# Kernel tuning notes

Hardware: AMD Instinct MI355X
Metric: run time of the kernel (lower is better)

## Reference

```python
import jax, jax.numpy as jnp
import numpy as np

N = 50000      # n_nodes
E = 800000     # n_edges (nnz)
F = 256        # n_features
H = 256        # architecture (GCN hidden)
K = 16         # n_clusters
CLUSTER_REG = 1.0
CON_REG = 1.0


def setup_inputs() -> dict:
    key = jax.random.key(0)
    ks = jax.random.split(key, 12)
    inp = {
        "edge_src": jax.random.randint(ks[0], (E,), 0, N, dtype=jnp.int32),
        "edge_dst": jax.random.randint(ks[1], (E,), 0, N, dtype=jnp.int32),
        "edge_w_norm": jax.random.uniform(ks[2], (E,), dtype=jnp.float32),
        "features": jax.random.normal(ks[3], (N, F), dtype=jnp.float32),
        "aug_features": jax.random.normal(ks[4], (N, F), dtype=jnp.float32),
        # GCN encoder params (Linear no-bias + additive bias per DGI-style GCN)
        "W1": jax.random.normal(ks[5], (F, H), dtype=jnp.float32) / np.sqrt(F),
        "b1": jnp.zeros((H,), dtype=jnp.float32),
        # student GCN params
        "Ws": jax.random.normal(ks[6], (H, K), dtype=jnp.float32) / np.sqrt(H),
        "bs": jnp.zeros((K,), dtype=jnp.float32),
        # teacher GCN params (EMA copy; fixed here)
        "Wt": jax.random.normal(ks[7], (H, K), dtype=jnp.float32) / np.sqrt(H),
        "bt": jnp.zeros((K,), dtype=jnp.float32),
        "n_nodes": N,
    }
    return inp


def _spmm(w, src, dst, X, n):
    # (sparse A) @ X with A given as COO (src=row, dst=col, w=value)
    return jax.ops.segment_sum(w[:, None] * X[dst], src, num_segments=n)


def _gcn(X, W, b, w, src, dst, n):
    # act(spmm(A_norm, X @ W) + b) with act = selu
    return jax.nn.selu(_spmm(w, src, dst, X @ W, n) + b)


def _normalize(x):
    # F.normalize(x, dim=-1, p=2)
    nrm = jnp.sqrt(jnp.sum(x * x, axis=-1, keepdims=True))
    return x / jnp.maximum(nrm, 1e-12)


def reference(edge_src, edge_dst, edge_w_norm, features, aug_features,
              W1, b1, Ws, bs, Wt, bt, n_nodes):
    n = features.shape[0]
    n_edges = edge_src.shape[0]

    # encoder + student assignments
    gcn_out = _gcn(features, W1, b1, edge_w_norm, edge_src, edge_dst, n)
    logits = _spmm(edge_w_norm, edge_src, edge_dst, gcn_out @ Ws, n) + bs
    assignments = jax.nn.softmax(jax.nn.selu(logits), axis=1)  # [N, K]

    # degrees = torch.sparse.sum(graph, dim=0) (binary adjacency values)
    ones_e = jnp.ones((n_edges,), dtype=features.dtype)
    degrees = jax.ops.segment_sum(ones_e, edge_dst, num_segments=n)[:, None]  # [N,1]

    # graph_pooled = (A @ S).T @ S  (A values are all 1)
    AS = jax.ops.segment_sum(assignments[edge_dst], edge_src, num_segments=n)
    graph_pooled = AS.T @ assignments  # [K, K]

    normalizer_left = assignments.T @ degrees          # [K, 1]
    normalizer = (normalizer_left @ normalizer_left.T) / 2.0 / n_edges
    spectral_loss = -jnp.trace(graph_pooled - normalizer) / 2.0 / n_edges

    cluster_sizes = jnp.sum(assignments, axis=0)
    cluster_loss = (jnp.linalg.norm(cluster_sizes) / n_nodes * np.sqrt(float(K)) - 1.0)
    cluster_loss = cluster_loss * CLUSTER_REG

    # teacher branch (no grad)
    g2 = _gcn(aug_features, W1, b1, edge_w_norm, edge_src, edge_dst, n)
    t_logits = _spmm(edge_w_norm, edge_src, edge_dst, g2 @ Wt, n) + bt
    assignments_hat = jax.lax.stop_gradient(
        jax.nn.softmax(jax.nn.selu(t_logits), axis=-1))

    con = jnp.mean(2.0 - 2.0 * jnp.sum(_normalize(assignments_hat) * _normalize(assignments), axis=-1))

    loss = spectral_loss + cluster_loss + CON_REG * con
    return loss
```

## Files before the change

kernel.cpp:

```cpp
#include <hip/hip_runtime.h>
#include <math.h>

constexpr int Fdim = 256;
constexpr int Hdim = 256;
constexpr int Kc   = 16;

constexpr int RSTRIDE = 32;
constexpr int NRED    = 34;
constexpr int BCAP    = 5120;

typedef __attribute__((ext_vector_type(8))) short s8v;
typedef __attribute__((ext_vector_type(4))) float f4v;

__device__ __forceinline__ float selu1(float x){
    const float scale = 1.0507009873554805f;
    const float alpha = 1.6732632423543772f;
    return scale * (x > 0.f ? x : alpha * expm1f(x));
}

__device__ __forceinline__ ushort f2bf(float x){
    union { float f; unsigned u; } c; c.f = x;
    unsigned r = c.u + 0x7fffu + ((c.u >> 16) & 1u);
    return (ushort)(r >> 16);
}

__device__ __forceinline__ float bflo(unsigned v){
    union { unsigned u; float f; } c; c.u = v << 16; return c.f;
}
__device__ __forceinline__ float bfhi(unsigned v){
    union { unsigned u; float f; } c; c.u = v & 0xffff0000u; return c.f;
}

__device__ __forceinline__ unsigned char f2fp8(float x){
    int v = __builtin_amdgcn_cvt_pk_fp8_f32(x, x, 0, false);
    return (unsigned char)(v & 0xff);
}

__global__ __launch_bounds__(256) void prep_kernel(
        const float* __restrict__ W1, ushort* __restrict__ WT,
        const float* __restrict__ Ws, const float* __restrict__ Wt,
        ushort* __restrict__ WsT, ushort* __restrict__ WtT){
    __shared__ float tbuf[16][17];
    int b = blockIdx.x;
    int t = threadIdx.x;
    if (b < 256){
        int bx = b & 15, by = b >> 4;
        int tx = t & 15, ty = t >> 4;
        int k  = by * 16 + ty;
        int nn = bx * 16 + tx;
        tbuf[ty][tx] = W1[k * 256 + nn];
        __syncthreads();
        int n2 = bx * 16 + ty;
        int k2 = by * 16 + tx;
        WT[n2 * 256 + k2] = f2bf(tbuf[tx][ty]);
    } else {
        int h = t;
        #pragma unroll
        for (int c = 0; c < 16; ++c){
            WsT[c * 256 + h] = f2bf(Ws[h * 16 + c]);
            WtT[c * 256 + h] = f2bf(Wt[h * 16 + c]);
        }
    }
}

__global__ __launch_bounds__(256, 2) void mega_kernel(
        const int* __restrict__ esrc, const int* __restrict__ edst,
        const float* __restrict__ ew, int* __restrict__ bcnt,
        int* __restrict__ bsrc, uint2* __restrict__ bdw, int E, int nbuck,
        const float* __restrict__ A0, const float* __restrict__ A1,
        const ushort* __restrict__ Bt, unsigned char* __restrict__ C8,
        int M, int nrt){
    __shared__ char smem[32768];
    int tid = threadIdx.x;

    if (blockIdx.x < 256){
        int* hist = (int*)smem;
        int* base = hist + 256;
        int* cur  = base + 256;
        int chunk = (E + 255) / 256;
        int lo = blockIdx.x * chunk;
        int hi = min(lo + chunk, E);
        hist[tid] = 0;
        __syncthreads();
        for (int i = lo + tid; i < hi; i += 256)
            atomicAdd(&hist[esrc[i] >> 8], 1);
        __syncthreads();
        if (tid < nbuck && hist[tid] > 0)
            base[tid] = atomicAdd(&bcnt[tid * 32], hist[tid]);
        cur[tid] = 0;
        __syncthreads();
        for (int i = lo + tid; i < hi; i += 256){
            int s = esrc[i], d = edst[i];
            float wv = ew[i];
            int b = s >> 8;
            int p = base[b] + atomicAdd(&cur[b], 1);
            if (p < BCAP){
                bsrc[(size_t)b * BCAP + p] = s;
                bdw[(size_t)b * BCAP + p]  = make_uint2((unsigned)d, __float_as_uint(wv));
            }
        }
        return;
    }

    ushort* blds = (ushort*)smem;
    int gid = blockIdx.x - 256;
    int z   = gid / (2 * nrt);
    int rem = gid - z * (2 * nrt);
    int by  = rem >> 1;
    int bx  = rem & 1;
    int n0  = bx * 128;
    int bm  = by * 128;
    const float* A = z ? A1 : A0;
    int halfoff = z * 256;

    int w = tid >> 6, l = tid & 63;
    int lr = l & 15, lk = l >> 4;

    int r0 = bm + w * 32 + lr;
    int r1 = r0 + 16;
    int rc0 = min(r0, M - 1), rc1 = min(r1, M - 1);

    f4v acc[2][8];
    #pragma unroll
    for (int m = 0; m < 2; ++m)
        #pragma unroll
        for (int t = 0; t < 8; ++t)
            acc[m][t] = (f4v){0.f, 0.f, 0.f, 0.f};

    for (int kp = 0; kp < 2; ++kp){
        #pragma unroll
        for (int j = 0; j < 8; ++j){
            int c  = j * 256 + tid;
            int nl = c >> 4, kc = c & 15;
            uint4 v = *reinterpret_cast<const uint4*>(
                Bt + (((size_t)(n0 + nl)) << 8) + kp * 128 + (kc << 3));
            unsigned boff = (unsigned)(((nl << 8) + (kc << 4)) ^ ((nl & 7) << 4));
            *reinterpret_cast<uint4*>(reinterpret_cast<char*>(blds) + boff) = v;
        }

        const float* a0 = A + (size_t)rc0 * 256 + kp * 128 + lk * 8;
        const float* a1 = A + (size_t)rc1 * 256 + kp * 128 + lk * 8;
        s8v af0[4], af1[4];
        #pragma unroll
        for (int ks = 0; ks < 4; ++ks){
            float4 x0 = *reinterpret_cast<const float4*>(a0 + ks * 32);
            float4 x1 = *reinterpret_cast<const float4*>(a0 + ks * 32 + 4);
            af0[ks][0] = (short)f2bf(x0.x); af0[ks][1] = (short)f2bf(x0.y);
            af0[ks][2] = (short)f2bf(x0.z); af0[ks][3] = (short)f2bf(x0.w);
            af0[ks][4] = (short)f2bf(x1.x); af0[ks][5] = (short)f2bf(x1.y);
            af0[ks][6] = (short)f2bf(x1.z); af0[ks][7] = (short)f2bf(x1.w);
            float4 y0 = *reinterpret_cast<const float4*>(a1 + ks * 32);
            float4 y1 = *reinterpret_cast<const float4*>(a1 + ks * 32 + 4);
            af1[ks][0] = (short)f2bf(y0.x); af1[ks][1] = (short)f2bf(y0.y);
            af1[ks][2] = (short)f2bf(y0.z); af1[ks][3] = (short)f2bf(y0.w);
            af1[ks][4] = (short)f2bf(y1.x); af1[ks][5] = (short)f2bf(y1.y);
            af1[ks][6] = (short)f2bf(y1.z); af1[ks][7] = (short)f2bf(y1.w);
        }
        __syncthreads();

        #pragma unroll
        for (int ks = 0; ks < 4; ++ks){
            #pragma unroll
            for (int t = 0; t < 8; ++t){
                int nl = t * 16 + lr;
                unsigned boff = (unsigned)(((nl << 8) + ((ks * 4 + lk) << 4)) ^ ((nl & 7) << 4));
                s8v bf = *reinterpret_cast<const s8v*>(reinterpret_cast<const char*>(blds) + boff);
                acc[0][t] = __builtin_amdgcn_mfma_f32_16x16x32_bf16(af0[ks], bf, acc[0][t], 0, 0, 0);
                acc[1][t] = __builtin_amdgcn_mfma_f32_16x16x32_bf16(af1[ks], bf, acc[1][t], 0, 0, 0);
            }
        }
        if (kp == 0) __syncthreads();
    }

    #pragma unroll
    for (int m = 0; m < 2; ++m){
        #pragma unroll
        for (int t = 0; t < 8; ++t){
            int col = n0 + t * 16 + lr;
            #pragma unroll
            for (int j = 0; j < 4; ++j){
                int row = bm + w * 32 + m * 16 + lk * 4 + j;
                if (row < M) C8[(size_t)row * 512 + halfoff + col] = f2fp8(acc[m][t][j]);
            }
        }
    }
}

__global__ __launch_bounds__(256) void csr_build_kernel(
        const int* __restrict__ bcnt,
        const int* __restrict__ bsrc, const uint2* __restrict__ bdw,
        int* __restrict__ roff, uint2* __restrict__ csr, int n, int nbuck){
    __shared__ int sb[256];
    __shared__ int hist[256];
    __shared__ int loc[256];
    __shared__ int cur[256];
    int b = blockIdx.x, t = threadIdx.x;

    int vb = (t < nbuck) ? min(bcnt[t * 32], BCAP) : 0;
    sb[t] = vb;
    __syncthreads();
    for (int off = 1; off < 256; off <<= 1){
        int x = (t >= off) ? sb[t - off] : 0;
        __syncthreads();
        sb[t] += x;
        __syncthreads();
    }
    if (b == 0 && t == 0) roff[n] = sb[nbuck - 1];
    int cnt  = min(bcnt[b * 32], BCAP);
    int base = sb[b] - cnt;
    __syncthreads();

    hist[t] = 0;
    __syncthreads();
    for (int i = t; i < cnt; i += 256)
        atomicAdd(&hist[bsrc[(size_t)b * BCAP + i] & 255], 1);
    __syncthreads();
    int v = hist[t];
    loc[t] = v;
    __syncthreads();
    for (int off = 1; off < 256; off <<= 1){
        int x = (t >= off) ? loc[t - off] : 0;
        __syncthreads();
        loc[t] += x;
        __syncthreads();
    }
    int gi = b * 256 + t;
    if (gi < n) roff[gi] = base + loc[t] - v;
    cur[t] = 0;
    __syncthreads();
    for (int i = t; i < cnt; i += 256){
        int s   = bsrc[(size_t)b * BCAP + i];
        int idx = s & 255;
        int p = base + (loc[idx] - hist[idx]) + atomicAdd(&cur[idx], 1);
        csr[p] = bdw[(size_t)b * BCAP + i];
    }
}

__global__ __launch_bounds__(256) void spmm_h2_kernel(
        const unsigned char* __restrict__ XWp,
        const int* __restrict__ roff, const uint2* __restrict__ csr,
        const float* __restrict__ b1,
        ushort* __restrict__ Gs, ushort* __restrict__ Gt, int n){
    int wid = threadIdx.x >> 6, lane = threadIdx.x & 63;
    int r = blockIdx.x * 4 + wid;
    if (r >= n) return;
    int half = lane >> 5;
    int hl   = lane & 31;
    const unsigned char* base = XWp + lane * 8;
    int e0 = roff[r], e1 = roff[r + 1];
    float acc[8] = {};

    #define ACCUM8(V, W) do{                                                      \
        auto fa_ = __builtin_amdgcn_cvt_pk_f32_fp8((V).x, false);                 \
        acc[0] = fmaf((W), fa_[0], acc[0]); acc[1] = fmaf((W), fa_[1], acc[1]);   \
        auto fb_ = __builtin_amdgcn_cvt_pk_f32_fp8((V).x, true);                  \
        acc[2] = fmaf((W), fb_[0], acc[2]); acc[3] = fmaf((W), fb_[1], acc[3]);   \
        auto fc_ = __builtin_amdgcn_cvt_pk_f32_fp8((V).y, false);                 \
        acc[4] = fmaf((W), fc_[0], acc[4]); acc[5] = fmaf((W), fc_[1], acc[5]);   \
        auto fd_ = __builtin_amdgcn_cvt_pk_f32_fp8((V).y, true);                  \
        acc[6] = fmaf((W), fd_[0], acc[6]); acc[7] = fmaf((W), fd_[1], acc[7]);   \
    }while(0)

    int e = e0;
    for (; e + 7 < e1; e += 8){
        uint2 c0 = csr[e],     c1 = csr[e + 1];
        uint2 c2 = csr[e + 2], c3 = csr[e + 3];
        uint2 c4 = csr[e + 4], c5 = csr[e + 5];
        uint2 c6 = csr[e + 6], c7 = csr[e + 7];
        uint2 v0 = *reinterpret_cast<const uint2*>(base + ((size_t)c0.x << 9));
        uint2 v1 = *reinterpret_cast<const uint2*>(base + ((size_t)c1.x << 9));
        uint2 v2 = *reinterpret_cast<const uint2*>(base + ((size_t)c2.x << 9));
        uint2 v3 = *reinterpret_cast<const uint2*>(base + ((size_t)c3.x << 9));
        uint2 v4 = *reinterpret_cast<const uint2*>(base + ((size_t)c4.x << 9));
        uint2 v5 = *reinterpret_cast<const uint2*>(base + ((size_t)c5.x << 9));
        uint2 v6 = *reinterpret_cast<const uint2*>(base + ((size_t)c6.x << 9));
        uint2 v7 = *reinterpret_cast<const uint2*>(base + ((size_t)c7.x << 9));
        ACCUM8(v0, __uint_as_float(c0.y)); ACCUM8(v1, __uint_as_float(c1.y));
        ACCUM8(v2, __uint_as_float(c2.y)); ACCUM8(v3, __uint_as_float(c3.y));
        ACCUM8(v4, __uint_as_float(c4.y)); ACCUM8(v5, __uint_as_float(c5.y));
        ACCUM8(v6, __uint_as_float(c6.y)); ACCUM8(v7, __uint_as_float(c7.y));
    }
    for (; e + 3 < e1; e += 4){
        uint2 c0 = csr[e],     c1 = csr[e + 1];
        uint2 c2 = csr[e + 2], c3 = csr[e + 3];
        uint2 v0 = *reinterpret_cast<const uint2*>(base + ((size_t)c0.x << 9));
        uint2 v1 = *reinterpret_cast<const uint2*>(base + ((size_t)c1.x << 9));
        uint2 v2 = *reinterpret_cast<const uint2*>(base + ((size_t)c2.x << 9));
        uint2 v3 = *reinterpret_cast<const uint2*>(base + ((size_t)c3.x << 9));
        ACCUM8(v0, __uint_as_float(c0.y)); ACCUM8(v1, __uint_as_float(c1.y));
        ACCUM8(v2, __uint_as_float(c2.y)); ACCUM8(v3, __uint_as_float(c3.y));
    }
    for (; e < e1; ++e){
        uint2 c = csr[e];
        uint2 v = *reinterpret_cast<const uint2*>(base + ((size_t)c.x << 9));
        ACCUM8(v, __uint_as_float(c.y));
    }
    #undef ACCUM8

    const float* bp = b1 + hl * 8;
    float4 bb0 = *reinterpret_cast<const float4*>(bp);
    float4 bb1 = *reinterpret_cast<const float4*>(bp + 4);
    float bv[8] = {bb0.x, bb0.y, bb0.z, bb0.w, bb1.x, bb1.y, bb1.z, bb1.w};
    ushort o[8];
    #pragma unroll
    for (int q = 0; q < 8; ++q) o[q] = f2bf(selu1(acc[q] + bv[q]));
    uint4 ov = *reinterpret_cast<const uint4*>(o);
    ushort* gout = (half ? Gt : Gs) + (size_t)r * Hdim + hl * 8;
    *reinterpret_cast<uint4*>(gout) = ov;
}

__global__ __launch_bounds__(256) void gemm_k2_kernel(
        const ushort* __restrict__ Gs, const ushort* __restrict__ Gt,
        const ushort* __restrict__ WsT, const ushort* __restrict__ WtT,
        unsigned* __restrict__ GSp, int n){
    int wv = blockIdx.x * 4 + (threadIdx.x >> 6);
    int l  = threadIdx.x & 63;
    int lr = l & 15, lk = l >> 4;
    int nw = (n + 15) >> 4;
    if (wv >= nw) return;
    int r0 = wv * 16;

    s8v bs_[8], bt_[8];
    #pragma unroll
    for (int ks = 0; ks < 8; ++ks){
        bs_[ks] = *reinterpret_cast<const s8v*>(WsT + lr * 256 + ks * 32 + lk * 8);
        bt_[ks] = *reinterpret_cast<const s8v*>(WtT + lr * 256 + ks * 32 + lk * 8);
    }

    f4v accs = (f4v){0.f,0.f,0.f,0.f}, acct = (f4v){0.f,0.f,0.f,0.f};
    int row = min(r0 + lr, n - 1);
    const ushort* gsrow = Gs + (size_t)row * 256 + lk * 8;
    const ushort* gtrow = Gt + (size_t)row * 256 + lk * 8;
    #pragma unroll
    for (int ks = 0; ks < 8; ++ks){
        s8v a_s = *reinterpret_cast<const s8v*>(gsrow + ks * 32);
        s8v a_t = *reinterpret_cast<const s8v*>(gtrow + ks * 32);
        accs = __builtin_amdgcn_mfma_f32_16x16x32_bf16(a_s, bs_[ks], accs, 0, 0, 0);
        acct = __builtin_amdgcn_mfma_f32_16x16x32_bf16(a_t, bt_[ks], acct, 0, 0, 0);
    }
    #pragma unroll
    for (int j = 0; j < 4; ++j){
        int rr = r0 + lk * 4 + j;
        if (rr < n){
            unsigned pv = (unsigned)f2bf(accs[j]) | ((unsigned)f2bf(acct[j]) << 16);
            GSp[(size_t)rr * 16 + lr] = pv;
        }
    }
}

__global__ __launch_bounds__(256) void spmm_k2_kernel(
        const unsigned* __restrict__ GSp,
        const int* __restrict__ roff, const uint2* __restrict__ csr,
        const float* __restrict__ bsv, const float* __restrict__ btv,
        float* __restrict__ asg, float* __restrict__ red, int n){
    int tid  = threadIdx.x;
    int wid  = tid >> 6, lane = tid & 63;
    int slot = lane >> 4, j = lane & 15;
    float bs_ = bsv[j], bt_ = btv[j];
    float cs_l = 0.f, con_l = 0.f;

    int rstride = gridDim.x * 4;
    for (int r = blockIdx.x * 4 + wid; r < n; r += rstride){
        int e0 = roff[r], e1 = roff[r + 1];
        float as_ = 0.f, at_ = 0.f;
        for (int e = e0 + slot; e < e1; e += 4){
            uint2 c = csr[e];
            float w = __uint_as_float(c.y);
            unsigned v = GSp[(size_t)c.x * 16 + j];
            as_ = fmaf(w, bflo(v), as_);
            at_ = fmaf(w, bfhi(v), at_);
        }
        as_ += __shfl_xor(as_, 16); as_ += __shfl_xor(as_, 32);
        at_ += __shfl_xor(at_, 16); at_ += __shfl_xor(at_, 32);
        float xs = selu1(as_ + bs_);
        float xt = selu1(at_ + bt_);
        float ms = xs, mt = xt;
        #pragma unroll
        for (int off = 8; off >= 1; off >>= 1){
            ms = fmaxf(ms, __shfl_xor(ms, off));
            mt = fmaxf(mt, __shfl_xor(mt, off));
        }
        float es = expf(xs - ms), et = expf(xt - mt);
        float ss = es, st = et;
        #pragma unroll
        for (int off = 8; off >= 1; off >>= 1){
            ss += __shfl_xor(ss, off);
            st += __shfl_xor(st, off);
        }
        float a = es / ss, b = et / st;
        if (slot == 0) asg[(size_t)r * 16 + j] = a;
        cs_l += a;
        float dot = a * b, na = a * a, nb = b * b;
        #pragma unroll
        for (int off = 8; off >= 1; off >>= 1){
            dot += __shfl_xor(dot, off);
            na  += __shfl_xor(na, off);
            nb  += __shfl_xor(nb, off);
        }
        if (j == 0){
            na = fmaxf(sqrtf(na), 1e-12f);
            nb = fmaxf(sqrtf(nb), 1e-12f);
            con_l += 2.f - 2.f * dot / (na * nb);
        }
    }

    cs_l  += __shfl_xor(cs_l, 16);  cs_l  += __shfl_xor(cs_l, 32);  cs_l  *= 0.25f;
    con_l += __shfl_xor(con_l, 16); con_l += __shfl_xor(con_l, 32); con_l *= 0.25f;

    __shared__ float part[4][17];
    if (lane < 16) part[wid][lane] = cs_l;
    if (lane == 0) part[wid][16]   = con_l;
    __syncthreads();
    if (tid < 16){
        float s = part[0][tid] + part[1][tid] + part[2][tid] + part[3][tid];
        atomicAdd(&red[(16 + tid) * RSTRIDE], s);
    } else if (tid == 16){
        float s = part[0][16] + part[1][16] + part[2][16] + part[3][16];
        atomicAdd(&red[32 * RSTRIDE], s);
    }
}

__global__ __launch_bounds__(256) void edge_trace_kernel(const int* __restrict__ src,
        const int* __restrict__ dst, const float* __restrict__ as_,
        float* __restrict__ red, int E){
    int tid    = blockIdx.x * blockDim.x + threadIdx.x;
    int stride = gridDim.x * blockDim.x;
    float dot = 0.f;
    float nl[16] = {};
    for (int i = tid; i < E; i += stride){
        const float4* pa = reinterpret_cast<const float4*>(as_ + (size_t)src[i] * 16);
        const float4* pb = reinterpret_cast<const float4*>(as_ + (size_t)dst[i] * 16);
        #pragma unroll
        for (int q = 0; q < 4; ++q){
            float4 va = pa[q]; float4 vb = pb[q];
            dot = fmaf(va.x, vb.x, dot); dot = fmaf(va.y, vb.y, dot);
            dot = fmaf(va.z, vb.z, dot); dot = fmaf(va.w, vb.w, dot);
            nl[q*4+0] += vb.x; nl[q*4+1] += vb.y;
            nl[q*4+2] += vb.z; nl[q*4+3] += vb.w;
        }
    }
    #pragma unroll
    for (int off = 1; off < 64; off <<= 1){
        dot += __shfl_xor(dot, off);
        #pragma unroll
        for (int k = 0; k < 16; ++k) nl[k] += __shfl_xor(nl[k], off);
    }
    __shared__ float part[4][17];
    int wid = threadIdx.x >> 6, lane = threadIdx.x & 63;
    if (lane == 0){
        #pragma unroll
        for (int k = 0; k < 16; ++k) part[wid][k] = nl[k];
        part[wid][16] = dot;
    }
    __syncthreads();
    int t = threadIdx.x;
    if (t < 16){
        float s = part[0][t] + part[1][t] + part[2][t] + part[3][t];
        atomicAdd(&red[t * RSTRIDE], s);
    } else if (t == 16){
        float s = part[0][16] + part[1][16] + part[2][16] + part[3][16];
        atomicAdd(&red[33 * RSTRIDE], s);
    }
}

__global__ void finalize_kernel(const float* __restrict__ red, float* __restrict__ out,
                                int n, int E){
    float trace = red[33 * RSTRIDE];
    float nl2 = 0.f, cs2 = 0.f;
    #pragma unroll
    for (int k = 0; k < 16; ++k){
        nl2 = fmaf(red[k * RSTRIDE],        red[k * RSTRIDE],        nl2);
        cs2 = fmaf(red[(16 + k) * RSTRIDE], red[(16 + k) * RSTRIDE], cs2);
    }
    float twoE = 2.f * (float)E;
    float spectral = -(trace - nl2 / twoE) / twoE;
    float cluster  = sqrtf(cs2) / (float)n * 4.f - 1.f;
    float con      = red[32 * RSTRIDE] / (float)n;
    out[0] = spectral + cluster + con;
}

extern "C" void kernel_launch(void* const* d_in, const int* in_sizes, int n_in,
                              void* d_out, int out_size, void* d_ws, size_t ws_size,
                              hipStream_t stream){
    const int*   esrc = (const int*)d_in[0];
    const int*   edst = (const int*)d_in[1];
    const float* ew   = (const float*)d_in[2];
    const float* feat = (const float*)d_in[3];
    const float* faug = (const float*)d_in[4];
    const float* W1   = (const float*)d_in[5];
    const float* b1   = (const float*)d_in[6];
    const float* Wsm  = (const float*)d_in[7];
    const float* bsv  = (const float*)d_in[8];
    const float* Wtm  = (const float*)d_in[9];
    const float* btv  = (const float*)d_in[10];
    int E = in_sizes[0];
    int N = in_sizes[3] / Fdim;

    char* ws = (char*)d_ws;
    size_t off = 0;
    auto alloc = [&](size_t bytes) -> char* {
        char* p = ws + off;
        off = (off + bytes + 255) & ~(size_t)255;
        return p;
    };
    int nbuck = (N + 255) >> 8;
    unsigned char* XWp = (unsigned char*)alloc((size_t)N * 512);
    ushort*   Gs    = (ushort*)alloc((size_t)N * Hdim * 2);
    ushort*   Gt    = (ushort*)alloc((size_t)N * Hdim * 2);
    unsigned* GSp   = (unsigned*)alloc((size_t)N * Kc * 4);
    float*    ASG_S = (float*)alloc((size_t)N * Kc * 4);
    ushort*   WT    = (ushort*)alloc((size_t)256 * 256 * 2);
    ushort*   WsT   = (ushort*)alloc((size_t)16 * 256 * 2);
    ushort*   WtT   = (ushort*)alloc((size_t)16 * 256 * 2);
    int*      ROFF  = (int*)alloc((size_t)(N + 1) * 4);
    int*      BCNT  = (int*)alloc((size_t)nbuck * 32 * 4);
    int*      BSRC  = (int*)alloc((size_t)nbuck * BCAP * 4);
    uint2*    BDW   = (uint2*)alloc((size_t)nbuck * BCAP * 8);
    uint2*    CSR8  = (uint2*)alloc((size_t)E * 8);
    float*    RED   = (float*)alloc((size_t)NRED * RSTRIDE * 4);

    hipMemsetAsync(BCNT, 0, (size_t)nbuck * 32 * 4, stream);
    hipMemsetAsync(RED, 0, (size_t)NRED * RSTRIDE * 4, stream);

    prep_kernel<<<257, 256, 0, stream>>>(W1, WT, Wsm, Wtm, WsT, WtT);

    int nrt = (N + 127) / 128;
    int mega_blocks = 256 + 2 * nrt * 2;
    mega_kernel<<<mega_blocks, 256, 0, stream>>>(esrc, edst, ew, BCNT, BSRC, BDW,
                                                 E, nbuck, feat, faug, WT, XWp,
                                                 N, nrt);

    csr_build_kernel<<<nbuck, 256, 0, stream>>>(BCNT, BSRC, BDW, CSR8 ? ROFF : ROFF,
                                                CSR8, N, nbuck);

    spmm_h2_kernel<<<(N + 3) / 4, 256, 0, stream>>>(XWp, ROFF, CSR8, b1, Gs, Gt, N);

    int nw = (N + 15) / 16;
    gemm_k2_kernel<<<(nw + 3) / 4, 256, 0, stream>>>(Gs, Gt, WsT, WtT, GSp, N);

    spmm_k2_kernel<<<2048, 256, 0, stream>>>(GSp, ROFF, CSR8, bsv, btv,
                                             ASG_S, RED, N);

    edge_trace_kernel<<<256, 256, 0, stream>>>(esrc, edst, ASG_S, RED, E);
    finalize_kernel<<<1, 1, 0, stream>>>(RED, (float*)d_out, N, E);
}
```

Before: 236.6 us.

## Store assignments as bf16, unroll gather loops, fold memsets into prep kernel

The softmax assignments are now stored as packed bf16 pairs instead of fp32, which halves the random-gather traffic in the edge trace kernel. Both the spmm_k2 edge loop and the edge trace loop are unrolled by two so more loads are in flight at once. The two hipMemsetAsync calls are replaced by zeroing inside extra blocks of the prep kernel, and the spmm_k2 grid is cut from 2048 to 1024 blocks. The cost is reduced precision in the spectral trace and normalizer terms.

```diff
diff --git a/kernel.cpp b/kernel.cpp
--- a/kernel.cpp
+++ b/kernel.cpp
@@ -39,7 +39,8 @@
 __global__ __launch_bounds__(256) void prep_kernel(
         const float* __restrict__ W1, ushort* __restrict__ WT,
         const float* __restrict__ Ws, const float* __restrict__ Wt,
-        ushort* __restrict__ WsT, ushort* __restrict__ WtT){
+        ushort* __restrict__ WsT, ushort* __restrict__ WtT,
+        float* __restrict__ red, int* __restrict__ bcnt, int nbuck){
     __shared__ float tbuf[16][17];
     int b = blockIdx.x;
     int t = threadIdx.x;
@@ -53,13 +54,16 @@
         int n2 = bx * 16 + ty;
         int k2 = by * 16 + tx;
         WT[n2 * 256 + k2] = f2bf(tbuf[tx][ty]);
-    } else {
+    } else if (b == 256){
         int h = t;
         #pragma unroll
         for (int c = 0; c < 16; ++c){
             WsT[c * 256 + h] = f2bf(Ws[h * 16 + c]);
             WtT[c * 256 + h] = f2bf(Wt[h * 16 + c]);
         }
+        for (int i = t; i < NRED * RSTRIDE; i += 256) red[i] = 0.f;
+    } else {
+        for (int i = t; i < nbuck * 32; i += 256) bcnt[i] = 0;
     }
 }
 
@@ -352,7 +356,7 @@
         const unsigned* __restrict__ GSp,
         const int* __restrict__ roff, const uint2* __restrict__ csr,
         const float* __restrict__ bsv, const float* __restrict__ btv,
-        float* __restrict__ asg, float* __restrict__ red, int n){
+        unsigned* __restrict__ asgh, float* __restrict__ red, int n){
     int tid  = threadIdx.x;
     int wid  = tid >> 6, lane = tid & 63;
     int slot = lane >> 4, j = lane & 15;
@@ -363,7 +367,17 @@
     for (int r = blockIdx.x * 4 + wid; r < n; r += rstride){
         int e0 = roff[r], e1 = roff[r + 1];
         float as_ = 0.f, at_ = 0.f;
-        for (int e = e0 + slot; e < e1; e += 4){
+        int e = e0 + slot;
+        for (; e + 4 < e1; e += 8){
+            uint2 c0 = csr[e];
+            uint2 c1 = csr[e + 4];
+            unsigned v0 = GSp[(size_t)c0.x * 16 + j];
+            unsigned v1 = GSp[(size_t)c1.x * 16 + j];
+            float w0 = __uint_as_float(c0.y), w1 = __uint_as_float(c1.y);
+            as_ = fmaf(w0, bflo(v0), as_); at_ = fmaf(w0, bfhi(v0), at_);
+            as_ = fmaf(w1, bflo(v1), as_); at_ = fmaf(w1, bfhi(v1), at_);
+        }
+        if (e < e1){
             uint2 c = csr[e];
             float w = __uint_as_float(c.y);
             unsigned v = GSp[(size_t)c.x * 16 + j];
@@ -388,7 +402,11 @@
             st += __shfl_xor(st, off);
         }
         float a = es / ss, b = et / st;
-        if (slot == 0) asg[(size_t)r * 16 + j] = a;
+        int d = lane & 7;
+        float alo = __shfl(a, 2 * d);
+        float ahi = __shfl(a, 2 * d + 1);
+        if (lane < 8)
+            asgh[(size_t)r * 8 + d] = (unsigned)f2bf(alo) | ((unsigned)f2bf(ahi) << 16);
         cs_l += a;
         float dot = a * b, na = a * a, nb = b * b;
         #pragma unroll
@@ -421,24 +439,42 @@
 }
 
 __global__ __launch_bounds__(256) void edge_trace_kernel(const int* __restrict__ src,
-        const int* __restrict__ dst, const float* __restrict__ as_,
+        const int* __restrict__ dst, const unsigned* __restrict__ asgh,
         float* __restrict__ red, int E){
     int tid    = blockIdx.x * blockDim.x + threadIdx.x;
     int stride = gridDim.x * blockDim.x;
     float dot = 0.f;
     float nl[16] = {};
-    for (int i = tid; i < E; i += stride){
-        const float4* pa = reinterpret_cast<const float4*>(as_ + (size_t)src[i] * 16);
-        const float4* pb = reinterpret_cast<const float4*>(as_ + (size_t)dst[i] * 16);
-        #pragma unroll
-        for (int q = 0; q < 4; ++q){
-            float4 va = pa[q]; float4 vb = pb[q];
-            dot = fmaf(va.x, vb.x, dot); dot = fmaf(va.y, vb.y, dot);
-            dot = fmaf(va.z, vb.z, dot); dot = fmaf(va.w, vb.w, dot);
-            nl[q*4+0] += vb.x; nl[q*4+1] += vb.y;
-            nl[q*4+2] += vb.z; nl[q*4+3] += vb.w;
-        }
-    }
+
+    #define EDGE(IA, IB) do{                                                     \
+        const uint4* pa_ = reinterpret_cast<const uint4*>(asgh + (size_t)(IA) * 8); \
+        const uint4* pb_ = reinterpret_cast<const uint4*>(asgh + (size_t)(IB) * 8); \
+        uint4 a0_ = pa_[0], a1_ = pa_[1];                                         \
+        uint4 b0_ = pb_[0], b1_ = pb_[1];                                         \
+        unsigned aa_[8] = {a0_.x,a0_.y,a0_.z,a0_.w,a1_.x,a1_.y,a1_.z,a1_.w};      \
+        unsigned bb_[8] = {b0_.x,b0_.y,b0_.z,b0_.w,b1_.x,b1_.y,b1_.z,b1_.w};      \
+        _Pragma("unroll")                                                         \
+        for (int q_ = 0; q_ < 8; ++q_){                                           \
+            float bl_ = bflo(bb_[q_]), bh_ = bfhi(bb_[q_]);                       \
+            dot = fmaf(bflo(aa_[q_]), bl_, dot);                                  \
+            dot = fmaf(bfhi(aa_[q_]), bh_, dot);                                  \
+            nl[2*q_]   += bl_;                                                    \
+            nl[2*q_+1] += bh_;                                                    \
+        } }while(0)
+
+    int i = tid;
+    for (; i + stride < E; i += 2 * stride){
+        int s0 = src[i], d0 = dst[i];
+        int s1 = src[i + stride], d1 = dst[i + stride];
+        EDGE(s0, d0);
+        EDGE(s1, d1);
+    }
+    if (i < E){
+        int s0 = src[i], d0 = dst[i];
+        EDGE(s0, d0);
+    }
+    #undef EDGE
+
     #pragma unroll
     for (int off = 1; off < 64; off <<= 1){
         dot += __shfl_xor(dot, off);
@@ -508,7 +544,7 @@
     ushort*   Gs    = (ushort*)alloc((size_t)N * Hdim * 2);
     ushort*   Gt    = (ushort*)alloc((size_t)N * Hdim * 2);
     unsigned* GSp   = (unsigned*)alloc((size_t)N * Kc * 4);
-    float*    ASG_S = (float*)alloc((size_t)N * Kc * 4);
+    unsigned* ASGH  = (unsigned*)alloc((size_t)N * 8 * 4);
     ushort*   WT    = (ushort*)alloc((size_t)256 * 256 * 2);
     ushort*   WsT   = (ushort*)alloc((size_t)16 * 256 * 2);
     ushort*   WtT   = (ushort*)alloc((size_t)16 * 256 * 2);
@@ -519,10 +555,7 @@
     uint2*    CSR8  = (uint2*)alloc((size_t)E * 8);
     float*    RED   = (float*)alloc((size_t)NRED * RSTRIDE * 4);
 
-    hipMemsetAsync(BCNT, 0, (size_t)nbuck * 32 * 4, stream);
-    hipMemsetAsync(RED, 0, (size_t)NRED * RSTRIDE * 4, stream);
-
-    prep_kernel<<<257, 256, 0, stream>>>(W1, WT, Wsm, Wtm, WsT, WtT);
+    prep_kernel<<<258, 256, 0, stream>>>(W1, WT, Wsm, Wtm, WsT, WtT, RED, BCNT, nbuck);
 
     int nrt = (N + 127) / 128;
     int mega_blocks = 256 + 2 * nrt * 2;
@@ -530,17 +563,16 @@
                                                  E, nbuck, feat, faug, WT, XWp,
                                                  N, nrt);
 
-    csr_build_kernel<<<nbuck, 256, 0, stream>>>(BCNT, BSRC, BDW, CSR8 ? ROFF : ROFF,
-                                                CSR8, N, nbuck);
+    csr_build_kernel<<<nbuck, 256, 0, stream>>>(BCNT, BSRC, BDW, ROFF, CSR8, N, nbuck);
 
     spmm_h2_kernel<<<(N + 3) / 4, 256, 0, stream>>>(XWp, ROFF, CSR8, b1, Gs, Gt, N);
 
     int nw = (N + 15) / 16;
     gemm_k2_kernel<<<(nw + 3) / 4, 256, 0, stream>>>(Gs, Gt, WsT, WtT, GSp, N);
 
-    spmm_k2_kernel<<<2048, 256, 0, stream>>>(GSp, ROFF, CSR8, bsv, btv,
-                                             ASG_S, RED, N);
-
-    edge_trace_kernel<<<256, 256, 0, stream>>>(esrc, edst, ASG_S, RED, E);
+    spmm_k2_kernel<<<1024, 256, 0, stream>>>(GSp, ROFF, CSR8, bsv, btv,
+                                             ASGH, RED, N);
+
+    edge_trace_kernel<<<256, 256, 0, stream>>>(esrc, edst, ASGH, RED, E);
     finalize_kernel<<<1, 1, 0, stream>>>(RED, (float*)d_out, N, E);
 }
```

After: 225.1 us. 1.05x faster.
